# Performance work log

Hardware: AMD Instinct MI355X
Metric: run time of the kernel (lower is better)

## Reference

```python
import jax, jax.numpy as jnp
import numpy as np

B, N, F, D, DB, C = 1024, 200000, 32, 128, 256, 96


def _ln(x, g, b, eps=1e-5):
    m = x.mean(-1, keepdims=True)
    v = ((x - m) ** 2).mean(-1, keepdims=True)
    return (x - m) / jnp.sqrt(v + eps) * g + b


def setup_inputs() -> dict:
    key = jax.random.key(0)
    ks = jax.random.split(key, 24)
    s = 0.05
    inp = {
        'x_num': jax.random.normal(ks[0], (B, F), jnp.float32),
        'cand_x_num': jax.random.normal(ks[1], (N, F), jnp.float32),
        'cand_y': jax.random.normal(ks[2], (N,), jnp.float32),
        'W_in': jax.random.normal(ks[3], (F, D), jnp.float32) * s,
        'b_in': jnp.zeros((D,), jnp.float32),
        'enc_w1': jax.random.normal(ks[4], (D, DB), jnp.float32) * s,
        'enc_b1': jnp.zeros((DB,), jnp.float32),
        'enc_w2': jax.random.normal(ks[5], (DB, D), jnp.float32) * s,
        'enc_b2': jnp.zeros((D,), jnp.float32),
        'ln_mix_g': jnp.ones((D,), jnp.float32),
        'ln_mix_b': jnp.zeros((D,), jnp.float32),
        'K_w': jax.random.normal(ks[6], (D, D), jnp.float32) * s,
        'K_b': jnp.zeros((D,), jnp.float32),
        'lab_w': jax.random.normal(ks[7], (1, D), jnp.float32) * s,
        'lab_b': jnp.zeros((D,), jnp.float32),
        'T_w1': jax.random.normal(ks[8], (D, DB), jnp.float32) * s,
        'T_b1': jnp.zeros((DB,), jnp.float32),
        'T_w2': jax.random.normal(ks[9], (DB, D), jnp.float32) * s,  # no bias
        'pred_ln_g': jnp.ones((D,), jnp.float32),
        'pred_ln_b': jnp.zeros((D,), jnp.float32),
        'pred_w1': jax.random.normal(ks[10], (D, DB), jnp.float32) * s,
        'pred_b1': jnp.zeros((DB,), jnp.float32),
        'pred_w2': jax.random.normal(ks[11], (DB, D), jnp.float32) * s,
        'pred_b2': jnp.zeros((D,), jnp.float32),
        'head_ln_g': jnp.ones((D,), jnp.float32),
        'head_ln_b': jnp.zeros((D,), jnp.float32),
        'head_w': jax.random.normal(ks[12], (D, 1), jnp.float32) * s,
        'head_b': jnp.zeros((1,), jnp.float32),
        'context_size': C,
    }
    return inp


def _forward(x_num, cand_x_num, cand_y, W_in, b_in, enc_w1, enc_b1, enc_w2, enc_b2,
             ln_mix_g, ln_mix_b, K_w, K_b, lab_w, lab_b, T_w1, T_b1, T_w2,
             pred_ln_g, pred_ln_b, pred_w1, pred_b1, pred_w2, pred_b2,
             head_ln_g, head_ln_b, head_w, head_b, context_size):
    def enc(z):
        h = z @ W_in + b_in                                   # [*, D]
        h = h + (jax.nn.relu(h @ enc_w1 + enc_b1) @ enc_w2 + enc_b2)
        k = _ln(h, ln_mix_g, ln_mix_b) @ K_w + K_b
        return h, k

    cand_k = enc(cand_x_num)[1]                               # [N, D]
    x, k = enc(x_num)                                         # [B, D]

    # brute-force kNN: negative squared L2 via matmul + square sums
    k2 = (k * k).sum(-1, keepdims=True)                       # [B, 1]
    ck2 = (cand_k * cand_k).sum(-1)                           # [N]
    sims = 2.0 * (k @ cand_k.T) - k2 - ck2[None, :]           # [B, N]
    _, idx = jax.lax.top_k(sims, context_size)                # [B, C]

    context_k = cand_k[idx]                                   # [B, C, D]
    sim_c = 2.0 * jnp.einsum('bd,bcd->bc', k, context_k) - k2 - (context_k ** 2).sum(-1)
    probs = jax.nn.softmax(sim_c, axis=-1)                    # [B, C]

    ctx_y = cand_y[idx][..., None] @ lab_w + lab_b            # [B, C, D]
    diff = k[:, None, :] - context_k                          # [B, C, D]
    vals = ctx_y + jax.nn.relu(diff @ T_w1 + T_b1) @ T_w2     # [B, C, D]
    context_x = jnp.einsum('bc,bcd->bd', probs, vals)         # [B, D]

    x = x + context_x
    h = _ln(x, pred_ln_g, pred_ln_b)
    x = x + (jax.nn.relu(h @ pred_w1 + pred_b1) @ pred_w2 + pred_b2)
    out = jax.nn.relu(_ln(x, head_ln_g, head_ln_b)) @ head_w + head_b
    return out                                                # [B, 1]


def reference(x_num, cand_x_num, cand_y, W_in, b_in, enc_w1, enc_b1, enc_w2, enc_b2,
              ln_mix_g, ln_mix_b, K_w, K_b, lab_w, lab_b, T_w1, T_b1, T_w2,
              pred_ln_g, pred_ln_b, pred_w1, pred_b1, pred_w2, pred_b2,
              head_ln_g, head_ln_b, head_w, head_b, context_size):
    return _forward(x_num, cand_x_num, cand_y, W_in, b_in, enc_w1, enc_b1, enc_w2, enc_b2,
                    ln_mix_g, ln_mix_b, K_w, K_b, lab_w, lab_b, T_w1, T_b1, T_w2,
                    pred_ln_g, pred_ln_b, pred_w1, pred_b1, pred_w2, pred_b2,
                    head_ln_g, head_ln_b, head_w, head_b, context_size)
```

## Files before the change

### kernel.cpp

```cpp
#include <hip/hip_runtime.h>
#include <hip/hip_bf16.h>

#define NC 200000
#define NCP 200064
#define NCT 1563
#define NRG 196
#define CTR 8
#define SCAP2 32
#define CROW (NRG * SCAP2)
#define SREG 25
#define BB 1024
#define DD 128
#define DBH 256
#define CS 96

typedef __attribute__((ext_vector_type(8))) short bf16x8;
typedef __attribute__((ext_vector_type(4))) float f32x4;

#define LDH 136
#define LDU 264

__device__ inline uint4 pack8(const float4 a, const float4 b) {
  union { __hip_bfloat16 h[8]; uint4 v; } r;
  r.h[0] = __float2bfloat16(a.x); r.h[1] = __float2bfloat16(a.y);
  r.h[2] = __float2bfloat16(a.z); r.h[3] = __float2bfloat16(a.w);
  r.h[4] = __float2bfloat16(b.x); r.h[5] = __float2bfloat16(b.y);
  r.h[6] = __float2bfloat16(b.z); r.h[7] = __float2bfloat16(b.w);
  return r.v;
}

__device__ inline unsigned encf(float v) {
  unsigned b = __float_as_uint(v);
  return (b & 0x80000000u) ? ~b : (b | 0x80000000u);
}
__device__ inline unsigned long long mkkey(float v, int idx) {
  unsigned u = encf(v);
  return (((unsigned long long)(~u)) << 32) | (unsigned)idx;
}

__device__ inline void gload16(const void* g, void* l) {
  __builtin_amdgcn_global_load_lds((const __attribute__((address_space(1))) void*)g,
                                   (__attribute__((address_space(3))) void*)l, 16, 0, 0);
}

__global__ __launch_bounds__(256) void k_prep(const float* __restrict__ w1,
                                              const float* __restrict__ w2,
                                              const float* __restrict__ kw,
                                              const float* __restrict__ tw1,
                                              __hip_bfloat16* __restrict__ w1t,
                                              __hip_bfloat16* __restrict__ w2t,
                                              __hip_bfloat16* __restrict__ kwt,
                                              __hip_bfloat16* __restrict__ tw1t) {
  const int i = blockIdx.x * 256 + threadIdx.x;
  if (i < 32768) {
    const int u = i >> 7, j = i & 127;
    w1t[i] = __float2bfloat16(w1[j * DBH + u]);
    tw1t[i] = __float2bfloat16(tw1[j * DBH + u]);
  }
  if (i < 32768) {
    const int d = i >> 8, u = i & 255;
    w2t[i] = __float2bfloat16(w2[u * DD + d]);
  }
  if (i < 16384) {
    const int d = i >> 7, j = i & 127;
    kwt[i] = __float2bfloat16(kw[j * DD + d]);
  }
}

__global__ __launch_bounds__(256) void k_pad(__hip_bfloat16* __restrict__ ckb16,
                                             float* __restrict__ ck2) {
  const int i = blockIdx.x * 256 + threadIdx.x;
  if (i < (NCP - NC) * DD) ckb16[(size_t)NC * DD + i] = __float2bfloat16(0.f);
  if (i < (NCP - NC)) ck2[NC + i] = 1e9f;
}

__global__ __launch_bounds__(256) void k_e1(const float* __restrict__ X,
                                            const float* __restrict__ W,
                                            const float* __restrict__ bias,
                                            float* __restrict__ H) {
  __shared__ float Xs[32 * 32];
  const int tid = threadIdx.x;
  const int r0 = blockIdx.x * 32;
  ((float4*)Xs)[tid] = ((const float4*)(X + (size_t)r0 * 32))[tid];
  __syncthreads();
  const int d0 = tid & 63;
  const int rh = tid >> 6;
  float acc0[8], acc1[8];
  const float b0 = bias[d0], b1 = bias[d0 + 64];
#pragma unroll
  for (int r = 0; r < 8; ++r) { acc0[r] = b0; acc1[r] = b1; }
#pragma unroll
  for (int k4 = 0; k4 < 8; ++k4) {
    float w0[4], w1[4];
#pragma unroll
    for (int kk = 0; kk < 4; ++kk) {
      w0[kk] = W[(k4 * 4 + kk) * DD + d0];
      w1[kk] = W[(k4 * 4 + kk) * DD + d0 + 64];
    }
#pragma unroll
    for (int r = 0; r < 8; ++r) {
      float4 x4 = ((const float4*)(Xs + (rh * 8 + r) * 32))[k4];
      acc0[r] += x4.x * w0[0] + x4.y * w0[1] + x4.z * w0[2] + x4.w * w0[3];
      acc1[r] += x4.x * w1[0] + x4.y * w1[1] + x4.z * w1[2] + x4.w * w1[3];
    }
  }
#pragma unroll
  for (int r = 0; r < 8; ++r) {
    const size_t row = (size_t)(r0 + rh * 8 + r);
    H[row * DD + d0] = acc0[r];
    H[row * DD + d0 + 64] = acc1[r];
  }
}

__global__ __launch_bounds__(256) void k_e23m(float* __restrict__ H,
                                              const __hip_bfloat16* __restrict__ W1t,
                                              const float* __restrict__ B1,
                                              const __hip_bfloat16* __restrict__ W2t,
                                              const float* __restrict__ B2) {
  __shared__ __hip_bfloat16 Hs[64 * LDH];
  __shared__ __hip_bfloat16 Us[64 * LDU];
  const int tid = threadIdx.x;
  const int r0 = blockIdx.x * 64;
#pragma unroll
  for (int i = 0; i < 4; ++i) {
    const int e8 = i * 256 + tid;
    const int row = e8 >> 4, c8 = e8 & 15;
    const float* src = H + (size_t)(r0 + row) * DD + c8 * 8;
    float4 f0 = *(const float4*)(src);
    float4 f1 = *(const float4*)(src + 4);
    *(uint4*)(Hs + row * LDH + c8 * 8) = pack8(f0, f1);
  }
  __syncthreads();
  const int l = tid & 63, w = tid >> 6;
  const int lr = l & 15, lg = l >> 4;
  {
    f32x4 acc[4][4] = {};
#pragma unroll
    for (int kk = 0; kk < 4; ++kk) {
      bf16x8 a[4], b[4];
#pragma unroll
      for (int mi = 0; mi < 4; ++mi)
        a[mi] = *(const bf16x8*)(Hs + (mi * 16 + lr) * LDH + kk * 32 + lg * 8);
#pragma unroll
      for (int ni = 0; ni < 4; ++ni)
        b[ni] = *(const bf16x8*)(W1t + (size_t)(w * 64 + ni * 16 + lr) * DD + kk * 32 + lg * 8);
#pragma unroll
      for (int mi = 0; mi < 4; ++mi)
#pragma unroll
        for (int ni = 0; ni < 4; ++ni)
          acc[mi][ni] = __builtin_amdgcn_mfma_f32_16x16x32_bf16(a[mi], b[ni], acc[mi][ni], 0, 0, 0);
    }
#pragma unroll
    for (int ni = 0; ni < 4; ++ni) {
      const int col = w * 64 + ni * 16 + lr;
      const float bb = B1[col];
#pragma unroll
      for (int mi = 0; mi < 4; ++mi)
#pragma unroll
        for (int r = 0; r < 4; ++r) {
          const int row = mi * 16 + lg * 4 + r;
          Us[row * LDU + col] = __float2bfloat16(fmaxf(acc[mi][ni][r] + bb, 0.f));
        }
    }
  }
  __syncthreads();
  {
    f32x4 acc[4][2] = {};
#pragma unroll
    for (int kk = 0; kk < 8; ++kk) {
      bf16x8 a[4], b[2];
#pragma unroll
      for (int mi = 0; mi < 4; ++mi)
        a[mi] = *(const bf16x8*)(Us + (mi * 16 + lr) * LDU + kk * 32 + lg * 8);
#pragma unroll
      for (int ni = 0; ni < 2; ++ni)
        b[ni] = *(const bf16x8*)(W2t + (size_t)(w * 32 + ni * 16 + lr) * DBH + kk * 32 + lg * 8);
#pragma unroll
      for (int mi = 0; mi < 4; ++mi)
#pragma unroll
        for (int ni = 0; ni < 2; ++ni)
          acc[mi][ni] = __builtin_amdgcn_mfma_f32_16x16x32_bf16(a[mi], b[ni], acc[mi][ni], 0, 0, 0);
    }
#pragma unroll
    for (int ni = 0; ni < 2; ++ni) {
      const int col = w * 32 + ni * 16 + lr;
      const float bb = B2[col];
#pragma unroll
      for (int mi = 0; mi < 4; ++mi)
#pragma unroll
        for (int r = 0; r < 4; ++r) {
          const int row = mi * 16 + lg * 4 + r;
          const size_t g = (size_t)(r0 + row) * DD + col;
          H[g] = H[g] + acc[mi][ni][r] + bb;
        }
    }
  }
}

__global__ __launch_bounds__(256) void k_e4m(const float* __restrict__ H,
                                             const float* __restrict__ g,
                                             const float* __restrict__ bln,
                                             const __hip_bfloat16* __restrict__ Kwt,
                                             const float* __restrict__ Kb,
                                             float* __restrict__ Kout,
                                             __hip_bfloat16* __restrict__ Kb16,
                                             float* __restrict__ k2out) {
  __shared__ __hip_bfloat16 Ls[64 * LDH];
  __shared__ float k2s[64];
  const int tid = threadIdx.x;
  const int r0 = blockIdx.x * 64;
  if (tid < 64) k2s[tid] = 0.f;
  {
    const int row = tid >> 2, q = tid & 3;
    const float* hr = H + (size_t)(r0 + row) * DD + q * 32;
    float v[32];
#pragma unroll
    for (int i = 0; i < 8; ++i) {
      float4 f = ((const float4*)hr)[i];
      v[i * 4 + 0] = f.x; v[i * 4 + 1] = f.y; v[i * 4 + 2] = f.z; v[i * 4 + 3] = f.w;
    }
    float s = 0.f;
#pragma unroll
    for (int i = 0; i < 32; ++i) s += v[i];
    s += __shfl_xor(s, 1); s += __shfl_xor(s, 2);
    const float mean = s * (1.f / 128.f);
    float vs = 0.f;
#pragma unroll
    for (int i = 0; i < 32; ++i) { float d = v[i] - mean; vs += d * d; }
    vs += __shfl_xor(vs, 1); vs += __shfl_xor(vs, 2);
    const float rstd = 1.f / sqrtf(vs * (1.f / 128.f) + 1e-5f);
#pragma unroll
    for (int i = 0; i < 4; ++i) {
      float t[8];
#pragma unroll
      for (int j = 0; j < 8; ++j) {
        const int col = q * 32 + i * 8 + j;
        t[j] = (v[i * 8 + j] - mean) * rstd * g[col] + bln[col];
      }
      float4 f0 = {t[0], t[1], t[2], t[3]}, f1 = {t[4], t[5], t[6], t[7]};
      *(uint4*)(Ls + row * LDH + q * 32 + i * 8) = pack8(f0, f1);
    }
  }
  __syncthreads();
  const int l = tid & 63, w = tid >> 6;
  const int lr = l & 15, lg = l >> 4;
  f32x4 acc[4][2] = {};
#pragma unroll
  for (int kk = 0; kk < 4; ++kk) {
    bf16x8 a[4], b[2];
#pragma unroll
    for (int mi = 0; mi < 4; ++mi)
      a[mi] = *(const bf16x8*)(Ls + (mi * 16 + lr) * LDH + kk * 32 + lg * 8);
#pragma unroll
    for (int ni = 0; ni < 2; ++ni)
      b[ni] = *(const bf16x8*)(Kwt + (size_t)(w * 32 + ni * 16 + lr) * DD + kk * 32 + lg * 8);
#pragma unroll
    for (int mi = 0; mi < 4; ++mi)
#pragma unroll
      for (int ni = 0; ni < 2; ++ni)
        acc[mi][ni] = __builtin_amdgcn_mfma_f32_16x16x32_bf16(a[mi], b[ni], acc[mi][ni], 0, 0, 0);
  }
  float p[4][4];
#pragma unroll
  for (int mi = 0; mi < 4; ++mi)
#pragma unroll
    for (int r = 0; r < 4; ++r) p[mi][r] = 0.f;
#pragma unroll
  for (int ni = 0; ni < 2; ++ni) {
    const int col = w * 32 + ni * 16 + lr;
    const float kb = Kb[col];
#pragma unroll
    for (int mi = 0; mi < 4; ++mi)
#pragma unroll
      for (int r = 0; r < 4; ++r) {
        const float val = acc[mi][ni][r] + kb;
        const int row = mi * 16 + lg * 4 + r;
        const size_t gg = (size_t)(r0 + row) * DD + col;
        Kout[gg] = val;
        Kb16[gg] = __float2bfloat16(val);
        p[mi][r] += val * val;
      }
  }
#pragma unroll
  for (int mi = 0; mi < 4; ++mi)
#pragma unroll
    for (int r = 0; r < 4; ++r) {
      float t = p[mi][r];
      t += __shfl_xor(t, 1); t += __shfl_xor(t, 2);
      t += __shfl_xor(t, 4); t += __shfl_xor(t, 8);
      if (lr == 0) atomicAdd(&k2s[mi * 16 + lg * 4 + r], t);
    }
  __syncthreads();
  if (tid < 64) k2out[r0 + tid] = k2s[tid];
}

__global__ __launch_bounds__(256) void k_simsA(const __hip_bfloat16* __restrict__ A,
                                               const __hip_bfloat16* __restrict__ Bm,
                                               const float* __restrict__ ck2,
                                               float* __restrict__ rmaxpart) {
  __shared__ __hip_bfloat16 Bs[128 * 128];
  __shared__ float part[2][128];
  const int tid = threadIdx.x;
  const int bid = blockIdx.x;
  const int gq = bid >> 6, rt = (bid >> 3) & 7, xq = bid & 7;
  const int range = gq * 8 + xq;
  if (range >= NRG) return;
  const int m0 = rt * 128;
  const int l = tid & 63, w = tid >> 6;
  const int wm = w >> 1, wn = w & 1;
  const int lr = l & 15, lg = l >> 4;
  bf16x8 a[4][4];
#pragma unroll
  for (int mi = 0; mi < 4; ++mi) {
    const __hip_bfloat16* ar = A + (size_t)(m0 + wm * 64 + mi * 16 + lr) * DD + lg * 8;
#pragma unroll
    for (int kk = 0; kk < 4; ++kk) a[mi][kk] = *(const bf16x8*)(ar + kk * 32);
  }
  float vmax[4][4];
#pragma unroll
  for (int mi = 0; mi < 4; ++mi)
#pragma unroll
    for (int r = 0; r < 4; ++r) vmax[mi][r] = -1e30f;
  for (int i = 0; i < CTR; ++i) {
    const int ct = range * CTR + i;
    if (ct >= NCT) break;
    const int n0 = ct * 128;
    {
      const char* gbase = (const char*)(Bm + (size_t)n0 * DD);
#pragma unroll
      for (int j = 0; j < 8; ++j) {
        const int r = w * 32 + j * 4 + (l >> 4);
        const int b = ((l & 15) * 16) ^ ((r & 7) << 4);
        gload16(gbase + (size_t)r * 256 + b, (char*)Bs + w * 8192 + j * 1024);
      }
    }
    float c2l[4];
#pragma unroll
    for (int ni = 0; ni < 4; ++ni) c2l[ni] = 0.5f * ck2[n0 + wn * 64 + ni * 16 + lr];
    __syncthreads();
    f32x4 acc[4][4] = {};
#pragma unroll
    for (int kk = 0; kk < 4; ++kk) {
      bf16x8 b[4];
#pragma unroll
      for (int ni = 0; ni < 4; ++ni) {
        const int row = wn * 64 + ni * 16 + lr;
        const int boff = (kk * 64 + lg * 16) ^ ((row & 7) << 4);
        b[ni] = *(const bf16x8*)((const char*)Bs + row * 256 + boff);
      }
#pragma unroll
      for (int mi = 0; mi < 4; ++mi)
#pragma unroll
        for (int ni = 0; ni < 4; ++ni)
          acc[mi][ni] = __builtin_amdgcn_mfma_f32_16x16x32_bf16(a[mi][kk], b[ni], acc[mi][ni], 0, 0, 0);
    }
#pragma unroll
    for (int mi = 0; mi < 4; ++mi)
#pragma unroll
      for (int r = 0; r < 4; ++r)
#pragma unroll
        for (int ni = 0; ni < 4; ++ni)
          vmax[mi][r] = fmaxf(vmax[mi][r], acc[mi][ni][r] - c2l[ni]);
    __syncthreads();
  }
#pragma unroll
  for (int mi = 0; mi < 4; ++mi)
#pragma unroll
    for (int r = 0; r < 4; ++r) {
      float v = vmax[mi][r];
#pragma unroll
      for (int mk = 1; mk < 16; mk <<= 1) v = fmaxf(v, __shfl_xor(v, mk));
      if (lr == 0) part[wn][wm * 64 + mi * 16 + lg * 4 + r] = v;
    }
  __syncthreads();
  if (tid < 128)
    rmaxpart[(size_t)range * BB + m0 + tid] = fmaxf(part[0][tid], part[1][tid]);
}

__global__ __launch_bounds__(256) void k_rmax(const float* __restrict__ rmaxpart,
                                              float* __restrict__ cutF) {
  const int row = blockIdx.x * 256 + threadIdx.x;
  float m = -1e30f;
  for (int j = 0; j < NRG; ++j) m = fmaxf(m, rmaxpart[(size_t)j * BB + row]);
  const float t = m - 7.0f;
  cutF[row] = t - (fabsf(t) + 8.0f) * 0.00390625f - 1e-5f;
}

__global__ __launch_bounds__(256) void k_simsB(const __hip_bfloat16* __restrict__ A,
                                               const __hip_bfloat16* __restrict__ Bm,
                                               const float* __restrict__ ck2,
                                               const float* __restrict__ cutF,
                                               unsigned long long* __restrict__ cand,
                                               int* __restrict__ cnt2) {
  __shared__ __hip_bfloat16 Bs[128 * 128];
  __shared__ float cut_s[128];
  __shared__ int lcnt[128];
  const int tid = threadIdx.x;
  const int bid = blockIdx.x;
  const int gq = bid >> 6, rt = (bid >> 3) & 7, xq = bid & 7;
  const int range = gq * 8 + xq;
  if (range >= NRG) return;
  const int m0 = rt * 128;
  if (tid < 128) { cut_s[tid] = cutF[m0 + tid]; lcnt[tid] = 0; }
  const int l = tid & 63, w = tid >> 6;
  const int wm = w >> 1, wn = w & 1;
  const int lr = l & 15, lg = l >> 4;
  bf16x8 a[4][4];
#pragma unroll
  for (int mi = 0; mi < 4; ++mi) {
    const __hip_bfloat16* ar = A + (size_t)(m0 + wm * 64 + mi * 16 + lr) * DD + lg * 8;
#pragma unroll
    for (int kk = 0; kk < 4; ++kk) a[mi][kk] = *(const bf16x8*)(ar + kk * 32);
  }
  for (int i = 0; i < CTR; ++i) {
    const int ct = range * CTR + i;
    if (ct >= NCT) break;
    const int n0 = ct * 128;
    {
      const char* gbase = (const char*)(Bm + (size_t)n0 * DD);
#pragma unroll
      for (int j = 0; j < 8; ++j) {
        const int r = w * 32 + j * 4 + (l >> 4);
        const int b = ((l & 15) * 16) ^ ((r & 7) << 4);
        gload16(gbase + (size_t)r * 256 + b, (char*)Bs + w * 8192 + j * 1024);
      }
    }
    float c2l[4];
#pragma unroll
    for (int ni = 0; ni < 4; ++ni) c2l[ni] = 0.5f * ck2[n0 + wn * 64 + ni * 16 + lr];
    __syncthreads();
    f32x4 acc[4][4] = {};
#pragma unroll
    for (int kk = 0; kk < 4; ++kk) {
      bf16x8 b[4];
#pragma unroll
      for (int ni = 0; ni < 4; ++ni) {
        const int row = wn * 64 + ni * 16 + lr;
        const int boff = (kk * 64 + lg * 16) ^ ((row & 7) << 4);
        b[ni] = *(const bf16x8*)((const char*)Bs + row * 256 + boff);
      }
#pragma unroll
      for (int mi = 0; mi < 4; ++mi)
#pragma unroll
        for (int ni = 0; ni < 4; ++ni)
          acc[mi][ni] = __builtin_amdgcn_mfma_f32_16x16x32_bf16(a[mi][kk], b[ni], acc[mi][ni], 0, 0, 0);
    }
#pragma unroll
    for (int ni = 0; ni < 4; ++ni) {
      const int gcol = n0 + wn * 64 + ni * 16 + lr;
#pragma unroll
      for (int mi = 0; mi < 4; ++mi)
#pragma unroll
        for (int r = 0; r < 4; ++r) {
          const int lrow = wm * 64 + mi * 16 + lg * 4 + r;
          const float x = acc[mi][ni][r] - c2l[ni];
          if (x >= cut_s[lrow]) {
            const float v = __bfloat162float(__float2bfloat16(x));
            const int q = atomicAdd(&lcnt[lrow], 1);
            if (q < SCAP2)
              cand[(size_t)(m0 + lrow) * CROW + range * SCAP2 + q] = mkkey(v, gcol);
          }
        }
    }
    __syncthreads();
  }
  if (tid < 128) {
    const int n = lcnt[tid];
    cnt2[(size_t)range * BB + m0 + tid] = n < SCAP2 ? n : SCAP2;
  }
}

__global__ __launch_bounds__(256) void k_sortB(const unsigned long long* __restrict__ cand,
                                               const int* __restrict__ cnt2,
                                               int* __restrict__ idx_out) {
  __shared__ unsigned long long keys[CROW];
  __shared__ int csum[NRG + 1];
  __shared__ int wred[40][4];
  __shared__ int outl[128];
  __shared__ int outc_sh;
  const int tid = threadIdx.x;
  const int wid = tid >> 6, lane = tid & 63;
  const int row = blockIdx.x;
  if (tid < NRG) csum[tid] = cnt2[(size_t)tid * BB + row];
  __syncthreads();
  if (tid == 0) {
    int s = 0;
    for (int j = 0; j < NRG; ++j) { const int c = csum[j]; csum[j] = s; s += c; }
    csum[NRG] = s;
  }
  __syncthreads();
  const int n = csum[NRG];
  if (tid < NRG) {
    const int base = csum[tid], c = csum[tid + 1] - base;
    const unsigned long long* src = cand + (size_t)row * CROW + tid * SCAP2;
    for (int j = 0; j < c; ++j) keys[base + j] = src[j];
  }
  __syncthreads();

  unsigned v16l[SREG];
  int idl[SREG];
#pragma unroll
  for (int s = 0; s < SREG; ++s) {
    const int i = tid + s * 256;
    if (i < n) {
      const unsigned long long k = keys[i];
      v16l[s] = (~(unsigned)(k >> 32)) >> 16;
      idl[s] = (int)(k & 0xFFFFFFFFu);
    } else {
      v16l[s] = 0u;
      idl[s] = 0x7FFFFFFF;
    }
  }

  int pass = 0;
  unsigned prefix = 0;
  int need = CS;
#pragma unroll
  for (int b = 15; b >= 0; --b) {
    int c1 = 0;
#pragma unroll
    for (int s = 0; s < SREG; ++s)
      c1 += ((v16l[s] >> (b + 1)) == prefix && ((v16l[s] >> b) & 1u)) ? 1 : 0;
#pragma unroll
    for (int d = 1; d < 64; d <<= 1) c1 += __shfl_xor(c1, d);
    if (lane == 0) wred[pass][wid] = c1;
    __syncthreads();
    const int cnt1 = wred[pass][0] + wred[pass][1] + wred[pass][2] + wred[pass][3];
    ++pass;
    if (need <= cnt1) prefix = (prefix << 1) | 1u;
    else { need -= cnt1; prefix = (prefix << 1); }
  }
  const unsigned V16star = prefix;

  unsigned iprefix = 0;
  int ineed = need;
#pragma unroll
  for (int b = 17; b >= 0; --b) {
    int c0 = 0;
#pragma unroll
    for (int s = 0; s < SREG; ++s)
      c0 += (v16l[s] == V16star && ((unsigned)idl[s] >> (b + 1)) == iprefix &&
             !(((unsigned)idl[s] >> b) & 1u)) ? 1 : 0;
#pragma unroll
    for (int d = 1; d < 64; d <<= 1) c0 += __shfl_xor(c0, d);
    if (lane == 0) wred[pass][wid] = c0;
    __syncthreads();
    const int cnt0 = wred[pass][0] + wred[pass][1] + wred[pass][2] + wred[pass][3];
    ++pass;
    if (ineed <= cnt0) iprefix = (iprefix << 1);
    else { ineed -= cnt0; iprefix = (iprefix << 1) | 1u; }
  }
  const unsigned ITstar = iprefix;

  if (tid == 0) outc_sh = 0;
  __syncthreads();
#pragma unroll
  for (int s = 0; s < SREG; ++s) {
    if (v16l[s] > V16star || (v16l[s] == V16star && (unsigned)idl[s] <= ITstar)) {
      const int q = atomicAdd(&outc_sh, 1);
      if (q < 128) outl[q] = idl[s];
    }
  }
  __syncthreads();
  const int ne = outc_sh;
  for (int i = tid; i < 128; i += 256)
    if (i >= ne) outl[i] = 0x7FFFFFFF;
  __syncthreads();
  for (int k = 2; k <= 128; k <<= 1) {
    for (int j = k >> 1; j > 0; j >>= 1) {
      if (tid < 128) {
        const int i = tid, ixj = i ^ j;
        if (ixj > i) {
          int a = outl[i], b = outl[ixj];
          const bool up = ((i & k) == 0);
          if ((a > b) == up) { outl[i] = b; outl[ixj] = a; }
        }
      }
      __syncthreads();
    }
  }
  if (tid < CS) {
    int id = outl[tid];
    if ((unsigned)id >= NC) id = 0;
    idx_out[row * CS + tid] = id;
  }
}

#define LDB 136
__global__ __launch_bounds__(256) void k_final(const float* __restrict__ XH,
                                               const float* __restrict__ XK,
                                               const float* __restrict__ CK,
                                               const float* __restrict__ CY,
                                               const int* __restrict__ IDX,
                                               const __hip_bfloat16* __restrict__ Tw1t,
                                               const float* __restrict__ Tb1,
                                               const float* __restrict__ Tw2,
                                               const float* __restrict__ labw,
                                               const float* __restrict__ labb,
                                               const float* __restrict__ pg,
                                               const float* __restrict__ pb,
                                               const float* __restrict__ pw1,
                                               const float* __restrict__ pb1,
                                               const float* __restrict__ pw2,
                                               const float* __restrict__ pb2,
                                               const float* __restrict__ hg,
                                               const float* __restrict__ hb,
                                               const float* __restrict__ hw,
                                               const float* __restrict__ hbias,
                                               float* __restrict__ OUT) {
  __shared__ float diffs[CS * 132];
  __shared__ int ids[CS];
  __shared__ float yv[CS], simc[CS], pr[CS];
  __shared__ float kv[DD], xv[DD];
  __shared__ float qs[DBH];
  __shared__ float xrow[DD], hln[DD], t2[DBH], x2[DD];
  __shared__ float red[DD];
  __shared__ float smv[1];
  const int tid = threadIdx.x;
  const int b = blockIdx.x;
  if (tid < CS) ids[tid] = IDX[b * CS + tid];
  if (tid < DD) { kv[tid] = XK[(size_t)b * DD + tid]; xv[tid] = XH[(size_t)b * DD + tid]; }
  __syncthreads();
  if (tid < CS) yv[tid] = CY[ids[tid]];
  for (int e = tid; e < CS * DD; e += 256) {
    const int c = e >> 7, j = e & 127;
    diffs[c * 132 + j] = kv[j] - CK[(size_t)ids[c] * DD + j];
  }
  __syncthreads();
  if (tid < CS) {
    float s = 0.f;
    for (int j = 0; j < DD; ++j) { float d = diffs[tid * 132 + j]; s -= d * d; }
    simc[tid] = s;
  }
  __syncthreads();
  if (tid < DD) red[tid] = (tid < CS) ? simc[tid] : -1e30f;
  __syncthreads();
  for (int s = 64; s > 0; s >>= 1) { if (tid < s) red[tid] = fmaxf(red[tid], red[tid + s]); __syncthreads(); }
  const float mx = red[0];
  __syncthreads();
  if (tid < DD) red[tid] = (tid < CS) ? expf(simc[tid] - mx) : 0.f;
  if (tid < CS) pr[tid] = expf(simc[tid] - mx);
  __syncthreads();
  for (int s = 64; s > 0; s >>= 1) { if (tid < s) red[tid] += red[tid + s]; __syncthreads(); }
  const float inv = 1.f / red[0];
  __syncthreads();
  if (tid < CS) pr[tid] *= inv;
  if (tid < DD) red[tid] = (tid < CS) ? pr[tid] * yv[tid] : 0.f;
  __syncthreads();
  for (int s = 64; s > 0; s >>= 1) { if (tid < s) red[tid] += red[tid + s]; __syncthreads(); }
  if (tid == 0) smv[0] = red[0];
  __hip_bfloat16* db16 = (__hip_bfloat16*)diffs;
  {
    float4 f0s[6], f1s[6];
#pragma unroll
    for (int i = 0; i < 6; ++i) {
      const int gidx = tid + 256 * i;
      const int row = gidx >> 4, c8 = gidx & 15;
      f0s[i] = *(const float4*)(diffs + row * 132 + c8 * 8);
      f1s[i] = *(const float4*)(diffs + row * 132 + c8 * 8 + 4);
    }
    __syncthreads();
#pragma unroll
    for (int i = 0; i < 6; ++i) {
      const int gidx = tid + 256 * i;
      const int row = gidx >> 4, c8 = gidx & 15;
      *(uint4*)(db16 + row * LDB + c8 * 8) = pack8(f0s[i], f1s[i]);
    }
  }
  __syncthreads();
  {
    const int w = tid >> 6, l = tid & 63;
    const int lr = l & 15, lg = l >> 4;
    const int u0 = w * 64;
    bf16x8 af[6][4];
#pragma unroll
    for (int mt = 0; mt < 6; ++mt)
#pragma unroll
      for (int k = 0; k < 4; ++k)
        af[mt][k] = *(const bf16x8*)(db16 + (mt * 16 + lr) * LDB + k * 32 + lg * 8);
#pragma unroll
    for (int nt = 0; nt < 4; ++nt) {
      const int u = u0 + nt * 16 + lr;
      bf16x8 bfr[4];
#pragma unroll
      for (int k = 0; k < 4; ++k)
        bfr[k] = *(const bf16x8*)(Tw1t + (size_t)u * DD + k * 32 + lg * 8);
      const float bb = Tb1[u];
      float qacc = 0.f;
#pragma unroll
      for (int mt = 0; mt < 6; ++mt) {
        f32x4 acc = {};
#pragma unroll
        for (int k = 0; k < 4; ++k)
          acc = __builtin_amdgcn_mfma_f32_16x16x32_bf16(af[mt][k], bfr[k], acc, 0, 0, 0);
#pragma unroll
        for (int r = 0; r < 4; ++r) {
          const int c = mt * 16 + lg * 4 + r;
          qacc += pr[c] * fmaxf(acc[r] + bb, 0.f);
        }
      }
      qacc += __shfl_xor(qacc, 16);
      qacc += __shfl_xor(qacc, 32);
      if (lg == 0) qs[u] = qacc;
    }
  }
  __syncthreads();
  if (tid < DD) {
    const int d = tid;
    float cx = smv[0] * labw[d] + labb[d];
    for (int u4 = 0; u4 < 64; ++u4) {
      float4 q4 = *(const float4*)(&qs[u4 * 4]);
      cx += q4.x * Tw2[(u4 * 4 + 0) * DD + d];
      cx += q4.y * Tw2[(u4 * 4 + 1) * DD + d];
      cx += q4.z * Tw2[(u4 * 4 + 2) * DD + d];
      cx += q4.w * Tw2[(u4 * 4 + 3) * DD + d];
    }
    xrow[d] = xv[d] + cx;
  }
  __syncthreads();
  if (tid < DD) red[tid] = xrow[tid];
  __syncthreads();
  for (int s = 64; s > 0; s >>= 1) { if (tid < s) red[tid] += red[tid + s]; __syncthreads(); }
  const float m1 = red[0] * (1.f / 128.f);
  __syncthreads();
  if (tid < DD) { float d = xrow[tid] - m1; red[tid] = d * d; }
  __syncthreads();
  for (int s = 64; s > 0; s >>= 1) { if (tid < s) red[tid] += red[tid + s]; __syncthreads(); }
  const float rstd1 = 1.f / sqrtf(red[0] * (1.f / 128.f) + 1e-5f);
  __syncthreads();
  if (tid < DD) hln[tid] = (xrow[tid] - m1) * rstd1 * pg[tid] + pb[tid];
  __syncthreads();
  {
    const int u = tid;
    float s = pb1[u];
    for (int j4 = 0; j4 < 32; ++j4) {
      float4 h4 = *(const float4*)(hln + j4 * 4);
      s += h4.x * pw1[(j4 * 4 + 0) * DBH + u];
      s += h4.y * pw1[(j4 * 4 + 1) * DBH + u];
      s += h4.z * pw1[(j4 * 4 + 2) * DBH + u];
      s += h4.w * pw1[(j4 * 4 + 3) * DBH + u];
    }
    t2[u] = fmaxf(s, 0.f);
  }
  __syncthreads();
  if (tid < DD) {
    const int d = tid;
    float s = pb2[d];
    for (int u4 = 0; u4 < 64; ++u4) {
      float4 t4 = *(const float4*)(t2 + u4 * 4);
      s += t4.x * pw2[(u4 * 4 + 0) * DD + d];
      s += t4.y * pw2[(u4 * 4 + 1) * DD + d];
      s += t4.z * pw2[(u4 * 4 + 2) * DD + d];
      s += t4.w * pw2[(u4 * 4 + 3) * DD + d];
    }
    x2[d] = xrow[d] + s;
  }
  __syncthreads();
  if (tid < DD) red[tid] = x2[tid];
  __syncthreads();
  for (int s = 64; s > 0; s >>= 1) { if (tid < s) red[tid] += red[tid + s]; __syncthreads(); }
  const float m2 = red[0] * (1.f / 128.f);
  __syncthreads();
  if (tid < DD) { float d = x2[tid] - m2; red[tid] = d * d; }
  __syncthreads();
  for (int s = 64; s > 0; s >>= 1) { if (tid < s) red[tid] += red[tid + s]; __syncthreads(); }
  const float rstd2 = 1.f / sqrtf(red[0] * (1.f / 128.f) + 1e-5f);
  __syncthreads();
  if (tid < DD) {
    float z = (x2[tid] - m2) * rstd2 * hg[tid] + hb[tid];
    z = fmaxf(z, 0.f);
    red[tid] = z * hw[tid];
  }
  __syncthreads();
  for (int s = 64; s > 0; s >>= 1) { if (tid < s) red[tid] += red[tid + s]; __syncthreads(); }
  if (tid == 0) OUT[b] = red[0] + hbias[0];
}

extern "C" void kernel_launch(void* const* d_in, const int* in_sizes, int n_in,
                              void* d_out, int out_size, void* d_ws, size_t ws_size,
                              hipStream_t stream) {
  (void)in_sizes; (void)n_in; (void)out_size; (void)ws_size;
  const float* x_num      = (const float*)d_in[0];
  const float* cand_x     = (const float*)d_in[1];
  const float* cand_y     = (const float*)d_in[2];
  const float* W_in       = (const float*)d_in[3];
  const float* b_in       = (const float*)d_in[4];
  const float* enc_w1     = (const float*)d_in[5];
  const float* enc_b1     = (const float*)d_in[6];
  const float* enc_w2     = (const float*)d_in[7];
  const float* enc_b2     = (const float*)d_in[8];
  const float* ln_mix_g   = (const float*)d_in[9];
  const float* ln_mix_b   = (const float*)d_in[10];
  const float* K_w        = (const float*)d_in[11];
  const float* K_b        = (const float*)d_in[12];
  const float* lab_w      = (const float*)d_in[13];
  const float* lab_b      = (const float*)d_in[14];
  const float* T_w1       = (const float*)d_in[15];
  const float* T_b1       = (const float*)d_in[16];
  const float* T_w2       = (const float*)d_in[17];
  const float* pred_ln_g  = (const float*)d_in[18];
  const float* pred_ln_b  = (const float*)d_in[19];
  const float* pred_w1    = (const float*)d_in[20];
  const float* pred_b1    = (const float*)d_in[21];
  const float* pred_w2    = (const float*)d_in[22];
  const float* pred_b2    = (const float*)d_in[23];
  const float* head_ln_g  = (const float*)d_in[24];
  const float* head_ln_b  = (const float*)d_in[25];
  const float* head_w     = (const float*)d_in[26];
  const float* head_b     = (const float*)d_in[27];
  float* out = (float*)d_out;

  char* w8 = (char*)d_ws;
  size_t off = 0;
  float* cand_k = (float*)(w8 + off);              off += (size_t)NC * DD * 4;
  float* cand_ck2 = (float*)(w8 + off);            off += (size_t)NCP * 4 + 256;
  float* xh = (float*)(w8 + off);                  off += (size_t)BB * DD * 4;
  float* xk = (float*)(w8 + off);                  off += (size_t)BB * DD * 4;
  float* xk2 = (float*)(w8 + off);                 off += 4096;
  __hip_bfloat16* xkb16 = (__hip_bfloat16*)(w8 + off); off += (size_t)BB * DD * 2;
  int* idx_all = (int*)(w8 + off);                 off += (size_t)BB * CS * 4;
  __hip_bfloat16* w1t = (__hip_bfloat16*)(w8 + off); off += (size_t)DBH * DD * 2;
  __hip_bfloat16* w2t = (__hip_bfloat16*)(w8 + off); off += (size_t)DD * DBH * 2;
  __hip_bfloat16* kwt = (__hip_bfloat16*)(w8 + off); off += (size_t)DD * DD * 2;
  __hip_bfloat16* tw1t = (__hip_bfloat16*)(w8 + off); off += (size_t)DBH * DD * 2;
  char* big = w8 + off;
  float* cand_h = (float*)big;
  unsigned long long* candb = (unsigned long long*)big;
  float* rmaxpart = (float*)(big + (size_t)56 * 1024 * 1024);
  int* cnt2 = (int*)(big + (size_t)57 * 1024 * 1024);
  float* cutF = (float*)(big + (size_t)58 * 1024 * 1024);
  __hip_bfloat16* ckb16 = (__hip_bfloat16*)(big + (size_t)NC * DD * 4);

  k_prep<<<128, 256, 0, stream>>>(enc_w1, enc_w2, K_w, T_w1, w1t, w2t, kwt, tw1t);
  k_pad<<<32, 256, 0, stream>>>(ckb16, cand_ck2);
  k_e1<<<NC / 32, 256, 0, stream>>>(cand_x, W_in, b_in, cand_h);
  k_e23m<<<NC / 64, 256, 0, stream>>>(cand_h, w1t, enc_b1, w2t, enc_b2);
  k_e4m<<<NC / 64, 256, 0, stream>>>(cand_h, ln_mix_g, ln_mix_b, kwt, K_b,
                                     cand_k, ckb16, cand_ck2);
  k_e1<<<BB / 32, 256, 0, stream>>>(x_num, W_in, b_in, xh);
  k_e23m<<<BB / 64, 256, 0, stream>>>(xh, w1t, enc_b1, w2t, enc_b2);
  k_e4m<<<BB / 64, 256, 0, stream>>>(xh, ln_mix_g, ln_mix_b, kwt, K_b,
                                     xk, xkb16, xk2);
  k_simsA<<<1600, 256, 0, stream>>>(xkb16, ckb16, cand_ck2, rmaxpart);
  k_rmax<<<4, 256, 0, stream>>>(rmaxpart, cutF);
  k_simsB<<<1600, 256, 0, stream>>>(xkb16, ckb16, cand_ck2, cutF, candb, cnt2);
  k_sortB<<<BB, 256, 0, stream>>>(candb, cnt2, idx_all);
  k_final<<<BB, 256, 0, stream>>>(xh, xk, cand_k, cand_y, idx_all,
                                  tw1t, T_b1, T_w2, lab_w, lab_b,
                                  pred_ln_g, pred_ln_b, pred_w1, pred_b1, pred_w2, pred_b2,
                                  head_ln_g, head_ln_b, head_w, head_b, out);
}
```

Measured before the change: 581.9 us.

## Restructure simsA to one candidate tile per block and parallelize row-max reduction

k_simsA now assigns one 128-candidate tile per block, loads that tile into LDS once, and loops over all 8 query row tiles. Per-row maxima are combined in shared memory with atomicMax on order-preserving encoded floats. The single 4-block k_rmax reduction is replaced by a 64-block partial reduction using global atomicMax plus a small finalize kernel, with a clear kernel added beforehand. The aim is to reuse B tiles across all query rows and to remove the serial reduction, at the cost of more rmaxpart traffic (1563 partial rows instead of 196) and extra kernel launches.

```diff
diff --git a/kernel.cpp b/kernel.cpp
--- a/kernel.cpp
+++ b/kernel.cpp
@@ -13,6 +13,7 @@
 #define DD 128
 #define DBH 256
 #define CS 96
+#define CTCH 98
 
 typedef __attribute__((ext_vector_type(8))) short bf16x8;
 typedef __attribute__((ext_vector_type(4))) float f32x4;
@@ -32,6 +33,9 @@
 __device__ inline unsigned encf(float v) {
   unsigned b = __float_as_uint(v);
   return (b & 0x80000000u) ? ~b : (b | 0x80000000u);
+}
+__device__ inline float decf(unsigned u) {
+  return __uint_as_float((u & 0x80000000u) ? (u ^ 0x80000000u) : ~u);
 }
 __device__ inline unsigned long long mkkey(float v, int idx) {
   unsigned u = encf(v);
@@ -299,45 +303,37 @@
                                                const float* __restrict__ ck2,
                                                float* __restrict__ rmaxpart) {
   __shared__ __hip_bfloat16 Bs[128 * 128];
-  __shared__ float part[2][128];
+  __shared__ unsigned vm[BB];
   const int tid = threadIdx.x;
-  const int bid = blockIdx.x;
-  const int gq = bid >> 6, rt = (bid >> 3) & 7, xq = bid & 7;
-  const int range = gq * 8 + xq;
-  if (range >= NRG) return;
-  const int m0 = rt * 128;
+  const int ct = blockIdx.x;
+  const int n0 = ct * 128;
   const int l = tid & 63, w = tid >> 6;
   const int wm = w >> 1, wn = w & 1;
   const int lr = l & 15, lg = l >> 4;
-  bf16x8 a[4][4];
-#pragma unroll
-  for (int mi = 0; mi < 4; ++mi) {
-    const __hip_bfloat16* ar = A + (size_t)(m0 + wm * 64 + mi * 16 + lr) * DD + lg * 8;
-#pragma unroll
-    for (int kk = 0; kk < 4; ++kk) a[mi][kk] = *(const bf16x8*)(ar + kk * 32);
-  }
-  float vmax[4][4];
-#pragma unroll
-  for (int mi = 0; mi < 4; ++mi)
-#pragma unroll
-    for (int r = 0; r < 4; ++r) vmax[mi][r] = -1e30f;
-  for (int i = 0; i < CTR; ++i) {
-    const int ct = range * CTR + i;
-    if (ct >= NCT) break;
-    const int n0 = ct * 128;
-    {
-      const char* gbase = (const char*)(Bm + (size_t)n0 * DD);
-#pragma unroll
-      for (int j = 0; j < 8; ++j) {
-        const int r = w * 32 + j * 4 + (l >> 4);
-        const int b = ((l & 15) * 16) ^ ((r & 7) << 4);
-        gload16(gbase + (size_t)r * 256 + b, (char*)Bs + w * 8192 + j * 1024);
-      }
-    }
-    float c2l[4];
-#pragma unroll
-    for (int ni = 0; ni < 4; ++ni) c2l[ni] = 0.5f * ck2[n0 + wn * 64 + ni * 16 + lr];
-    __syncthreads();
+#pragma unroll
+  for (int i = 0; i < 4; ++i) vm[i * 256 + tid] = 0u;
+  {
+    const char* gbase = (const char*)(Bm + (size_t)n0 * DD);
+#pragma unroll
+    for (int j = 0; j < 8; ++j) {
+      const int r = w * 32 + j * 4 + (l >> 4);
+      const int b = ((l & 15) * 16) ^ ((r & 7) << 4);
+      gload16(gbase + (size_t)r * 256 + b, (char*)Bs + w * 8192 + j * 1024);
+    }
+  }
+  float c2l[4];
+#pragma unroll
+  for (int ni = 0; ni < 4; ++ni) c2l[ni] = 0.5f * ck2[n0 + wn * 64 + ni * 16 + lr];
+  __syncthreads();
+  for (int rt = 0; rt < 8; ++rt) {
+    const int m0 = rt * 128;
+    bf16x8 a[4][4];
+#pragma unroll
+    for (int mi = 0; mi < 4; ++mi) {
+      const __hip_bfloat16* ar = A + (size_t)(m0 + wm * 64 + mi * 16 + lr) * DD + lg * 8;
+#pragma unroll
+      for (int kk = 0; kk < 4; ++kk) a[mi][kk] = *(const bf16x8*)(ar + kk * 32);
+    }
     f32x4 acc[4][4] = {};
 #pragma unroll
     for (int kk = 0; kk < 4; ++kk) {
@@ -357,32 +353,46 @@
 #pragma unroll
     for (int mi = 0; mi < 4; ++mi)
 #pragma unroll
-      for (int r = 0; r < 4; ++r)
-#pragma unroll
-        for (int ni = 0; ni < 4; ++ni)
-          vmax[mi][r] = fmaxf(vmax[mi][r], acc[mi][ni][r] - c2l[ni]);
-    __syncthreads();
-  }
-#pragma unroll
-  for (int mi = 0; mi < 4; ++mi)
-#pragma unroll
-    for (int r = 0; r < 4; ++r) {
-      float v = vmax[mi][r];
-#pragma unroll
-      for (int mk = 1; mk < 16; mk <<= 1) v = fmaxf(v, __shfl_xor(v, mk));
-      if (lr == 0) part[wn][wm * 64 + mi * 16 + lg * 4 + r] = v;
-    }
-  __syncthreads();
-  if (tid < 128)
-    rmaxpart[(size_t)range * BB + m0 + tid] = fmaxf(part[0][tid], part[1][tid]);
-}
-
-__global__ __launch_bounds__(256) void k_rmax(const float* __restrict__ rmaxpart,
-                                              float* __restrict__ cutF) {
+      for (int r = 0; r < 4; ++r) {
+        float v = -1e30f;
+#pragma unroll
+        for (int ni = 0; ni < 4; ++ni) v = fmaxf(v, acc[mi][ni][r] - c2l[ni]);
+#pragma unroll
+        for (int mk = 1; mk < 16; mk <<= 1) v = fmaxf(v, __shfl_xor(v, mk));
+        if (lr == 0)
+          atomicMax(&vm[m0 + wm * 64 + mi * 16 + lg * 4 + r], encf(v));
+      }
+  }
+  __syncthreads();
+#pragma unroll
+  for (int i = 0; i < 4; ++i) {
+    const int row = i * 256 + tid;
+    rmaxpart[(size_t)ct * BB + row] = decf(vm[row]);
+  }
+}
+
+__global__ __launch_bounds__(256) void k_clearR(unsigned* __restrict__ rmaxE) {
+  const int tid = threadIdx.x;
+#pragma unroll
+  for (int i = 0; i < 4; ++i) rmaxE[i * 256 + tid] = 0u;
+}
+
+__global__ __launch_bounds__(256) void k_rmaxP(const float* __restrict__ rmaxpart,
+                                               unsigned* __restrict__ rmaxE) {
+  const int bid = blockIdx.x;
+  const int rc = bid & 3, jc = bid >> 2;
+  const int row = rc * 256 + threadIdx.x;
+  const int j0 = jc * CTCH;
+  const int j1 = (j0 + CTCH < NCT) ? j0 + CTCH : NCT;
+  float m = -1e30f;
+  for (int j = j0; j < j1; ++j) m = fmaxf(m, rmaxpart[(size_t)j * BB + row]);
+  atomicMax(&rmaxE[row], encf(m));
+}
+
+__global__ __launch_bounds__(256) void k_rmaxF(const unsigned* __restrict__ rmaxE,
+                                               float* __restrict__ cutF) {
   const int row = blockIdx.x * 256 + threadIdx.x;
-  float m = -1e30f;
-  for (int j = 0; j < NRG; ++j) m = fmaxf(m, rmaxpart[(size_t)j * BB + row]);
-  const float t = m - 7.0f;
+  const float t = decf(rmaxE[row]) - 7.0f;
   cutF[row] = t - (fabsf(t) + 8.0f) * 0.00390625f - 1e-5f;
 }
 
@@ -827,8 +837,9 @@
   float* cand_h = (float*)big;
   unsigned long long* candb = (unsigned long long*)big;
   float* rmaxpart = (float*)(big + (size_t)56 * 1024 * 1024);
-  int* cnt2 = (int*)(big + (size_t)57 * 1024 * 1024);
-  float* cutF = (float*)(big + (size_t)58 * 1024 * 1024);
+  unsigned* rmaxE = (unsigned*)(big + (size_t)63 * 1024 * 1024);
+  int* cnt2 = (int*)(big + (size_t)64 * 1024 * 1024);
+  float* cutF = (float*)(big + (size_t)65 * 1024 * 1024);
   __hip_bfloat16* ckb16 = (__hip_bfloat16*)(big + (size_t)NC * DD * 4);
 
   k_prep<<<128, 256, 0, stream>>>(enc_w1, enc_w2, K_w, T_w1, w1t, w2t, kwt, tw1t);
@@ -841,8 +852,10 @@
   k_e23m<<<BB / 64, 256, 0, stream>>>(xh, w1t, enc_b1, w2t, enc_b2);
   k_e4m<<<BB / 64, 256, 0, stream>>>(xh, ln_mix_g, ln_mix_b, kwt, K_b,
                                      xk, xkb16, xk2);
-  k_simsA<<<1600, 256, 0, stream>>>(xkb16, ckb16, cand_ck2, rmaxpart);
-  k_rmax<<<4, 256, 0, stream>>>(rmaxpart, cutF);
+  k_clearR<<<1, 256, 0, stream>>>(rmaxE);
+  k_simsA<<<NCT, 256, 0, stream>>>(xkb16, ckb16, cand_ck2, rmaxpart);
+  k_rmaxP<<<64, 256, 0, stream>>>(rmaxpart, rmaxE);
+  k_rmaxF<<<4, 256, 0, stream>>>(rmaxE, cutF);
   k_simsB<<<1600, 256, 0, stream>>>(xkb16, ckb16, cand_ck2, cutF, candb, cnt2);
   k_sortB<<<BB, 256, 0, stream>>>(candb, cnt2, idx_all);
   k_final<<<BB, 256, 0, stream>>>(xh, xk, cand_k, cand_y, idx_all,
```

Measured after the change: 659.1 us. 13.3% more time.

## Fuse candidate encoder stages into one kernel keeping activations in registers

Applied to the files above, without the earlier changes.

Merges the input projection, the residual MLP block, the LayerNorm and the K projection into a single kernel per 64-row tile. Intermediate activations stay in registers and shared memory instead of round-tripping a 200000x128 fp32 buffer through global memory three times. The LayerNorm statistics are now computed by cross-wave shared-memory reductions, which adds several block barriers and increases shared-memory and register use per block. A decf helper is also added but not used.

```diff
diff --git a/kernel.cpp b/kernel.cpp
--- a/kernel.cpp
+++ b/kernel.cpp
@@ -32,6 +32,9 @@
 __device__ inline unsigned encf(float v) {
   unsigned b = __float_as_uint(v);
   return (b & 0x80000000u) ? ~b : (b | 0x80000000u);
+}
+__device__ inline float decf(unsigned u) {
+  return __uint_as_float((u & 0x80000000u) ? (u ^ 0x80000000u) : ~u);
 }
 __device__ inline unsigned long long mkkey(float v, int idx) {
   unsigned u = encf(v);
@@ -74,65 +77,67 @@
   if (i < (NCP - NC)) ck2[NC + i] = 1e9f;
 }
 
-__global__ __launch_bounds__(256) void k_e1(const float* __restrict__ X,
-                                            const float* __restrict__ W,
-                                            const float* __restrict__ bias,
-                                            float* __restrict__ H) {
-  __shared__ float Xs[32 * 32];
-  const int tid = threadIdx.x;
-  const int r0 = blockIdx.x * 32;
-  ((float4*)Xs)[tid] = ((const float4*)(X + (size_t)r0 * 32))[tid];
-  __syncthreads();
-  const int d0 = tid & 63;
-  const int rh = tid >> 6;
-  float acc0[8], acc1[8];
-  const float b0 = bias[d0], b1 = bias[d0 + 64];
-#pragma unroll
-  for (int r = 0; r < 8; ++r) { acc0[r] = b0; acc1[r] = b1; }
-#pragma unroll
-  for (int k4 = 0; k4 < 8; ++k4) {
-    float w0[4], w1[4];
-#pragma unroll
-    for (int kk = 0; kk < 4; ++kk) {
-      w0[kk] = W[(k4 * 4 + kk) * DD + d0];
-      w1[kk] = W[(k4 * 4 + kk) * DD + d0 + 64];
-    }
-#pragma unroll
-    for (int r = 0; r < 8; ++r) {
-      float4 x4 = ((const float4*)(Xs + (rh * 8 + r) * 32))[k4];
-      acc0[r] += x4.x * w0[0] + x4.y * w0[1] + x4.z * w0[2] + x4.w * w0[3];
-      acc1[r] += x4.x * w1[0] + x4.y * w1[1] + x4.z * w1[2] + x4.w * w1[3];
-    }
-  }
-#pragma unroll
-  for (int r = 0; r < 8; ++r) {
-    const size_t row = (size_t)(r0 + rh * 8 + r);
-    H[row * DD + d0] = acc0[r];
-    H[row * DD + d0 + 64] = acc1[r];
-  }
-}
-
-__global__ __launch_bounds__(256) void k_e23m(float* __restrict__ H,
+__global__ __launch_bounds__(256) void k_encf(const float* __restrict__ X,
+                                              const float* __restrict__ Win,
+                                              const float* __restrict__ bin,
                                               const __hip_bfloat16* __restrict__ W1t,
                                               const float* __restrict__ B1,
                                               const __hip_bfloat16* __restrict__ W2t,
-                                              const float* __restrict__ B2) {
+                                              const float* __restrict__ B2,
+                                              const float* __restrict__ g,
+                                              const float* __restrict__ bln,
+                                              const __hip_bfloat16* __restrict__ Kwt,
+                                              const float* __restrict__ Kb,
+                                              float* __restrict__ Kout,
+                                              __hip_bfloat16* __restrict__ Kb16,
+                                              float* __restrict__ k2out,
+                                              float* __restrict__ Hout) {
+  __shared__ float Xs[64 * 36];
+  __shared__ float Ws[32 * 128];
   __shared__ __hip_bfloat16 Hs[64 * LDH];
   __shared__ __hip_bfloat16 Us[64 * LDU];
+  __shared__ float redS[4 * 64];
+  __shared__ float k2s[64];
   const int tid = threadIdx.x;
   const int r0 = blockIdx.x * 64;
-#pragma unroll
-  for (int i = 0; i < 4; ++i) {
-    const int e8 = i * 256 + tid;
-    const int row = e8 >> 4, c8 = e8 & 15;
-    const float* src = H + (size_t)(r0 + row) * DD + c8 * 8;
-    float4 f0 = *(const float4*)(src);
-    float4 f1 = *(const float4*)(src + 4);
-    *(uint4*)(Hs + row * LDH + c8 * 8) = pack8(f0, f1);
-  }
-  __syncthreads();
   const int l = tid & 63, w = tid >> 6;
   const int lr = l & 15, lg = l >> 4;
+  if (tid < 64) k2s[tid] = 0.f;
+  {
+    const float4* gx = (const float4*)(X + (size_t)r0 * 32);
+#pragma unroll
+    for (int i = 0; i < 2; ++i) {
+      const int e4 = tid + 256 * i;
+      const int row = e4 >> 3, c4 = e4 & 7;
+      ((float4*)Xs)[row * 9 + c4] = gx[e4];
+    }
+    const float4* gw = (const float4*)Win;
+#pragma unroll
+    for (int i = 0; i < 4; ++i) ((float4*)Ws)[tid + 256 * i] = gw[tid + 256 * i];
+  }
+  __syncthreads();
+  float Hreg[4][4][2];
+#pragma unroll
+  for (int ni = 0; ni < 2; ++ni) {
+    const int col = w * 32 + ni * 16 + lr;
+    const float bb = bin[col];
+    float wc[32];
+#pragma unroll
+    for (int k = 0; k < 32; ++k) wc[k] = Ws[k * 128 + col];
+#pragma unroll
+    for (int mi = 0; mi < 4; ++mi)
+#pragma unroll
+      for (int r = 0; r < 4; ++r) {
+        const int row = mi * 16 + lg * 4 + r;
+        const float* xr = Xs + row * 36;
+        float s = bb;
+#pragma unroll
+        for (int k = 0; k < 32; ++k) s += xr[k] * wc[k];
+        Hreg[mi][r][ni] = s;
+        Hs[row * LDH + col] = __float2bfloat16(s);
+      }
+  }
+  __syncthreads();
   {
     f32x4 acc[4][4] = {};
 #pragma unroll
@@ -150,6 +155,7 @@
         for (int ni = 0; ni < 4; ++ni)
           acc[mi][ni] = __builtin_amdgcn_mfma_f32_16x16x32_bf16(a[mi], b[ni], acc[mi][ni], 0, 0, 0);
     }
+    __syncthreads();
 #pragma unroll
     for (int ni = 0; ni < 4; ++ni) {
       const int col = w * 64 + ni * 16 + lr;
@@ -183,113 +189,128 @@
     }
 #pragma unroll
     for (int ni = 0; ni < 2; ++ni) {
+      const float bb = B2[w * 32 + ni * 16 + lr];
+#pragma unroll
+      for (int mi = 0; mi < 4; ++mi)
+#pragma unroll
+        for (int r = 0; r < 4; ++r)
+          Hreg[mi][r][ni] += acc[mi][ni][r] + bb;
+    }
+  }
+  if (Hout) {
+#pragma unroll
+    for (int ni = 0; ni < 2; ++ni) {
       const int col = w * 32 + ni * 16 + lr;
-      const float bb = B2[col];
-#pragma unroll
-      for (int mi = 0; mi < 4; ++mi)
-#pragma unroll
-        for (int r = 0; r < 4; ++r) {
-          const int row = mi * 16 + lg * 4 + r;
-          const size_t g = (size_t)(r0 + row) * DD + col;
-          H[g] = H[g] + acc[mi][ni][r] + bb;
-        }
-    }
-  }
-}
-
-__global__ __launch_bounds__(256) void k_e4m(const float* __restrict__ H,
-                                             const float* __restrict__ g,
-                                             const float* __restrict__ bln,
-                                             const __hip_bfloat16* __restrict__ Kwt,
-                                             const float* __restrict__ Kb,
-                                             float* __restrict__ Kout,
-                                             __hip_bfloat16* __restrict__ Kb16,
-                                             float* __restrict__ k2out) {
-  __shared__ __hip_bfloat16 Ls[64 * LDH];
-  __shared__ float k2s[64];
-  const int tid = threadIdx.x;
-  const int r0 = blockIdx.x * 64;
-  if (tid < 64) k2s[tid] = 0.f;
-  {
-    const int row = tid >> 2, q = tid & 3;
-    const float* hr = H + (size_t)(r0 + row) * DD + q * 32;
-    float v[32];
-#pragma unroll
-    for (int i = 0; i < 8; ++i) {
-      float4 f = ((const float4*)hr)[i];
-      v[i * 4 + 0] = f.x; v[i * 4 + 1] = f.y; v[i * 4 + 2] = f.z; v[i * 4 + 3] = f.w;
-    }
-    float s = 0.f;
-#pragma unroll
-    for (int i = 0; i < 32; ++i) s += v[i];
-    s += __shfl_xor(s, 1); s += __shfl_xor(s, 2);
-    const float mean = s * (1.f / 128.f);
-    float vs = 0.f;
-#pragma unroll
-    for (int i = 0; i < 32; ++i) { float d = v[i] - mean; vs += d * d; }
-    vs += __shfl_xor(vs, 1); vs += __shfl_xor(vs, 2);
-    const float rstd = 1.f / sqrtf(vs * (1.f / 128.f) + 1e-5f);
-#pragma unroll
-    for (int i = 0; i < 4; ++i) {
-      float t[8];
-#pragma unroll
-      for (int j = 0; j < 8; ++j) {
-        const int col = q * 32 + i * 8 + j;
-        t[j] = (v[i * 8 + j] - mean) * rstd * g[col] + bln[col];
-      }
-      float4 f0 = {t[0], t[1], t[2], t[3]}, f1 = {t[4], t[5], t[6], t[7]};
-      *(uint4*)(Ls + row * LDH + q * 32 + i * 8) = pack8(f0, f1);
-    }
-  }
-  __syncthreads();
-  const int l = tid & 63, w = tid >> 6;
-  const int lr = l & 15, lg = l >> 4;
-  f32x4 acc[4][2] = {};
-#pragma unroll
-  for (int kk = 0; kk < 4; ++kk) {
-    bf16x8 a[4], b[2];
-#pragma unroll
-    for (int mi = 0; mi < 4; ++mi)
-      a[mi] = *(const bf16x8*)(Ls + (mi * 16 + lr) * LDH + kk * 32 + lg * 8);
-#pragma unroll
-    for (int ni = 0; ni < 2; ++ni)
-      b[ni] = *(const bf16x8*)(Kwt + (size_t)(w * 32 + ni * 16 + lr) * DD + kk * 32 + lg * 8);
-#pragma unroll
-    for (int mi = 0; mi < 4; ++mi)
-#pragma unroll
-      for (int ni = 0; ni < 2; ++ni)
-        acc[mi][ni] = __builtin_amdgcn_mfma_f32_16x16x32_bf16(a[mi], b[ni], acc[mi][ni], 0, 0, 0);
-  }
-  float p[4][4];
+#pragma unroll
+      for (int mi = 0; mi < 4; ++mi)
+#pragma unroll
+        for (int r = 0; r < 4; ++r)
+          Hout[(size_t)(r0 + mi * 16 + lg * 4 + r) * DD + col] = Hreg[mi][r][ni];
+    }
+  }
+  __syncthreads();
+  float mean_[4][4], rstd_[4][4];
 #pragma unroll
   for (int mi = 0; mi < 4; ++mi)
 #pragma unroll
-    for (int r = 0; r < 4; ++r) p[mi][r] = 0.f;
+    for (int r = 0; r < 4; ++r) {
+      float ps = Hreg[mi][r][0] + Hreg[mi][r][1];
+      ps += __shfl_xor(ps, 1); ps += __shfl_xor(ps, 2);
+      ps += __shfl_xor(ps, 4); ps += __shfl_xor(ps, 8);
+      if (lr == 0) redS[w * 64 + mi * 16 + lg * 4 + r] = ps;
+    }
+  __syncthreads();
+#pragma unroll
+  for (int mi = 0; mi < 4; ++mi)
+#pragma unroll
+    for (int r = 0; r < 4; ++r) {
+      const int row = mi * 16 + lg * 4 + r;
+      mean_[mi][r] = (redS[row] + redS[64 + row] + redS[128 + row] + redS[192 + row]) * (1.f / 128.f);
+    }
+  __syncthreads();
+#pragma unroll
+  for (int mi = 0; mi < 4; ++mi)
+#pragma unroll
+    for (int r = 0; r < 4; ++r) {
+      const float d0 = Hreg[mi][r][0] - mean_[mi][r];
+      const float d1 = Hreg[mi][r][1] - mean_[mi][r];
+      float ps = d0 * d0 + d1 * d1;
+      ps += __shfl_xor(ps, 1); ps += __shfl_xor(ps, 2);
+      ps += __shfl_xor(ps, 4); ps += __shfl_xor(ps, 8);
+      if (lr == 0) redS[w * 64 + mi * 16 + lg * 4 + r] = ps;
+    }
+  __syncthreads();
+#pragma unroll
+  for (int mi = 0; mi < 4; ++mi)
+#pragma unroll
+    for (int r = 0; r < 4; ++r) {
+      const int row = mi * 16 + lg * 4 + r;
+      const float v = (redS[row] + redS[64 + row] + redS[128 + row] + redS[192 + row]) * (1.f / 128.f);
+      rstd_[mi][r] = 1.f / sqrtf(v + 1e-5f);
+    }
+  __hip_bfloat16* Ls = Us;
 #pragma unroll
   for (int ni = 0; ni < 2; ++ni) {
     const int col = w * 32 + ni * 16 + lr;
-    const float kb = Kb[col];
+    const float gc = g[col], bc = bln[col];
 #pragma unroll
     for (int mi = 0; mi < 4; ++mi)
 #pragma unroll
       for (int r = 0; r < 4; ++r) {
-        const float val = acc[mi][ni][r] + kb;
         const int row = mi * 16 + lg * 4 + r;
-        const size_t gg = (size_t)(r0 + row) * DD + col;
-        Kout[gg] = val;
-        Kb16[gg] = __float2bfloat16(val);
-        p[mi][r] += val * val;
+        const float val = (Hreg[mi][r][ni] - mean_[mi][r]) * rstd_[mi][r] * gc + bc;
+        Ls[row * LDH + col] = __float2bfloat16(val);
       }
   }
-#pragma unroll
-  for (int mi = 0; mi < 4; ++mi)
-#pragma unroll
-    for (int r = 0; r < 4; ++r) {
-      float t = p[mi][r];
-      t += __shfl_xor(t, 1); t += __shfl_xor(t, 2);
-      t += __shfl_xor(t, 4); t += __shfl_xor(t, 8);
-      if (lr == 0) atomicAdd(&k2s[mi * 16 + lg * 4 + r], t);
-    }
+  __syncthreads();
+  {
+    f32x4 acc[4][2] = {};
+#pragma unroll
+    for (int kk = 0; kk < 4; ++kk) {
+      bf16x8 a[4], b[2];
+#pragma unroll
+      for (int mi = 0; mi < 4; ++mi)
+        a[mi] = *(const bf16x8*)(Ls + (mi * 16 + lr) * LDH + kk * 32 + lg * 8);
+#pragma unroll
+      for (int ni = 0; ni < 2; ++ni)
+        b[ni] = *(const bf16x8*)(Kwt + (size_t)(w * 32 + ni * 16 + lr) * DD + kk * 32 + lg * 8);
+#pragma unroll
+      for (int mi = 0; mi < 4; ++mi)
+#pragma unroll
+        for (int ni = 0; ni < 2; ++ni)
+          acc[mi][ni] = __builtin_amdgcn_mfma_f32_16x16x32_bf16(a[mi], b[ni], acc[mi][ni], 0, 0, 0);
+    }
+    float p[4][4];
+#pragma unroll
+    for (int mi = 0; mi < 4; ++mi)
+#pragma unroll
+      for (int r = 0; r < 4; ++r) p[mi][r] = 0.f;
+#pragma unroll
+    for (int ni = 0; ni < 2; ++ni) {
+      const int col = w * 32 + ni * 16 + lr;
+      const float kb = Kb[col];
+#pragma unroll
+      for (int mi = 0; mi < 4; ++mi)
+#pragma unroll
+        for (int r = 0; r < 4; ++r) {
+          const float val = acc[mi][ni][r] + kb;
+          const int row = mi * 16 + lg * 4 + r;
+          const size_t gg = (size_t)(r0 + row) * DD + col;
+          Kout[gg] = val;
+          Kb16[gg] = __float2bfloat16(val);
+          p[mi][r] += val * val;
+        }
+    }
+#pragma unroll
+    for (int mi = 0; mi < 4; ++mi)
+#pragma unroll
+      for (int r = 0; r < 4; ++r) {
+        float t = p[mi][r];
+        t += __shfl_xor(t, 1); t += __shfl_xor(t, 2);
+        t += __shfl_xor(t, 4); t += __shfl_xor(t, 8);
+        if (lr == 0) atomicAdd(&k2s[mi * 16 + lg * 4 + r], t);
+      }
+  }
   __syncthreads();
   if (tid < 64) k2out[r0 + tid] = k2s[tid];
 }
@@ -824,7 +845,6 @@
   __hip_bfloat16* kwt = (__hip_bfloat16*)(w8 + off); off += (size_t)DD * DD * 2;
   __hip_bfloat16* tw1t = (__hip_bfloat16*)(w8 + off); off += (size_t)DBH * DD * 2;
   char* big = w8 + off;
-  float* cand_h = (float*)big;
   unsigned long long* candb = (unsigned long long*)big;
   float* rmaxpart = (float*)(big + (size_t)56 * 1024 * 1024);
   int* cnt2 = (int*)(big + (size_t)57 * 1024 * 1024);
@@ -833,14 +853,12 @@
 
   k_prep<<<128, 256, 0, stream>>>(enc_w1, enc_w2, K_w, T_w1, w1t, w2t, kwt, tw1t);
   k_pad<<<32, 256, 0, stream>>>(ckb16, cand_ck2);
-  k_e1<<<NC / 32, 256, 0, stream>>>(cand_x, W_in, b_in, cand_h);
-  k_e23m<<<NC / 64, 256, 0, stream>>>(cand_h, w1t, enc_b1, w2t, enc_b2);
-  k_e4m<<<NC / 64, 256, 0, stream>>>(cand_h, ln_mix_g, ln_mix_b, kwt, K_b,
-                                     cand_k, ckb16, cand_ck2);
-  k_e1<<<BB / 32, 256, 0, stream>>>(x_num, W_in, b_in, xh);
-  k_e23m<<<BB / 64, 256, 0, stream>>>(xh, w1t, enc_b1, w2t, enc_b2);
-  k_e4m<<<BB / 64, 256, 0, stream>>>(xh, ln_mix_g, ln_mix_b, kwt, K_b,
-                                     xk, xkb16, xk2);
+  k_encf<<<NC / 64, 256, 0, stream>>>(cand_x, W_in, b_in, w1t, enc_b1, w2t, enc_b2,
+                                      ln_mix_g, ln_mix_b, kwt, K_b,
+                                      cand_k, ckb16, cand_ck2, nullptr);
+  k_encf<<<BB / 64, 256, 0, stream>>>(x_num, W_in, b_in, w1t, enc_b1, w2t, enc_b2,
+                                      ln_mix_g, ln_mix_b, kwt, K_b,
+                                      xk, xkb16, xk2, xh);
   k_simsA<<<1600, 256, 0, stream>>>(xkb16, ckb16, cand_ck2, rmaxpart);
   k_rmax<<<4, 256, 0, stream>>>(rmaxpart, cutF);
   k_simsB<<<1600, 256, 0, stream>>>(xkb16, ckb16, cand_ck2, cutF, candb, cnt2);
```

After: 677.3 us. 16.4% more time.
